# Optimization experiments

Hardware: AMD Instinct MI355X
Metric: run time of the kernel (lower is better)

## Reference

```python
import jax, jax.numpy as jnp
import numpy as np

EPS = 1e-08


def setup_inputs() -> dict:
    key = jax.random.key(0)
    k1, k2 = jax.random.split(key)
    z = jax.random.normal(k1, (32, 768, 32, 32), dtype=jnp.float32)
    memory = jax.random.normal(k2, (512, 768), dtype=jnp.float32)
    return {"z": z, "memory": memory}


def _l2_normalize(x, axis=-1, eps=1e-12):
    # Matches torch F.normalize(dim=-1): x / max(||x||, eps)
    n = jnp.sqrt(jnp.sum(x * x, axis=axis, keepdims=True))
    return x / jnp.maximum(n, eps)


def reference(z, memory):
    B, C, H, W = z.shape
    M = memory.shape[0]
    # (B, C, H, W) -> (B, H*W, C)
    z_flat = jnp.transpose(z, (0, 2, 3, 1)).reshape(B, H * W, C)
    z_norm = _l2_normalize(z_flat)
    mem_norm = _l2_normalize(memory)
    # cosine-similarity scores: (B, N, M)
    scores = jnp.einsum('bnc,mc->bnm', z_norm, mem_norm)
    w = jax.nn.softmax(scores, axis=-1)
    lam = 1.0 / M
    # hard-shrink sparsification: relu(w - lam) * w / (|w - lam| + eps)
    d = w - lam
    attn_w = jax.nn.relu(d) * w / (jnp.abs(d) + EPS)
    attn_w = attn_w / (jnp.sum(attn_w, axis=-1, keepdims=True) + EPS)
    # weighted readout against the RAW (un-normalized) memory
    z_hat_flat = jnp.einsum('bnm,mc->bnc', attn_w, memory)
    z_hat = jnp.transpose(z_hat_flat.reshape(B, H, W, C), (0, 3, 1, 2))
    return (z_hat, attn_w)
```

## Files before the change

### kernel.cpp

```cpp
#include <hip/hip_runtime.h>
#include <hip/hip_bf16.h>
#include <math.h>

typedef short short8 __attribute__((ext_vector_type(8)));
typedef float f32x4 __attribute__((ext_vector_type(4)));
typedef _Float16 f16x8 __attribute__((ext_vector_type(8)));

#define CC 768
#define NN 1024
#define RR 32768
#define MM 512
#define ZSTRIDE 786432
#define OUT_ATTN_OFF 25165824
#define SPLIT_SC 2048.0f
#define INV_SC   (1.0f / 2048.0f)

static __device__ __forceinline__ short f2bf(float f) {
    __hip_bfloat16 h = __float2bfloat16(f);
    return *reinterpret_cast<short*>(&h);
}

static __device__ __forceinline__ double fast_exp_neg(double x) {
    const double LOG2E = 1.4426950408889634074;
    const double LN2   = 0.6931471805599453094;
    const double MAGIC = 6755399441055744.0;
    double t = x * LOG2E;
    double c = t + MAGIC;
    double n = c - MAGIC;
    int ni = (int)__double2loint(c);
    double g = (t - n) * LN2;
    double r = 2.505210838544172e-08;
    r = fma(r, g, 2.755731922398589e-07);
    r = fma(r, g, 2.7557319223985893e-06);
    r = fma(r, g, 2.48015873015873e-05);
    r = fma(r, g, 1.984126984126984e-04);
    r = fma(r, g, 1.388888888888889e-03);
    r = fma(r, g, 8.333333333333333e-03);
    r = fma(r, g, 4.1666666666666664e-02);
    r = fma(r, g, 1.6666666666666666e-01);
    r = fma(r, g, 0.5);
    r = fma(r, g, 1.0);
    r = fma(r, g, 1.0);
    double sc = __hiloint2double((1023 + ni) << 20, 0);
    return r * sc;
}

static __device__ __forceinline__ double fast_rcp(double x) {
    double r = (double)(1.0f / (float)x);
    r = r * (2.0 - x * r);
    r = r * (2.0 - x * r);
    return r;
}

__global__ __launch_bounds__(256) void prep_mem_kernel(const float* __restrict__ memory,
                                                       _Float16* __restrict__ mem_h,
                                                       _Float16* __restrict__ mem_L,
                                                       short* __restrict__ memT_bf) {
    int m = blockIdx.x;
    int t = threadIdx.x;
    double ss = 0.0;
    for (int c = t; c < CC; c += 256) {
        float v = memory[m * CC + c];
        ss += (double)v * (double)v;
    }
    #pragma unroll
    for (int off = 32; off > 0; off >>= 1) ss += __shfl_xor(ss, off);
    __shared__ double red[4];
    __shared__ double invs;
    if ((t & 63) == 0) red[t >> 6] = ss;
    __syncthreads();
    if (t == 0) {
        double tot = red[0] + red[1] + red[2] + red[3];
        invs = 1.0 / fmax(sqrt(tot), 1e-12);
    }
    __syncthreads();
    float inv = (float)invs;
    for (int c = t; c < CC; c += 256) {
        float v  = memory[m * CC + c];
        float nv = v * inv;
        _Float16 h = (_Float16)nv;
        float r1 = nv - (float)h;
        mem_h[m * CC + c] = h;
        mem_L[m * CC + c] = (_Float16)(r1 * SPLIT_SC);
        memT_bf[c * MM + m] = f2bf(v);
    }
}

#define SWZ(row_, k_) ((((row_) << 5) + (k_)) ^ (((row_) & 7) << 3))
__global__ __launch_bounds__(512, 4) void scores_gemm_kernel(const float* __restrict__ z,
                                                             const _Float16* __restrict__ mem_h,
                                                             const _Float16* __restrict__ mem_L,
                                                             float* __restrict__ out_scores,
                                                             double* __restrict__ zinv_ws) {
    __shared__ _Float16 AT[2][2][4096];
    __shared__ _Float16 BT[2][2][4096];
    __shared__ double ssred[512];

    const int t    = threadIdx.x;
    const int lane = t & 63;
    const int wv   = t >> 6;
    const int lrow = lane & 15;
    const int gk   = lane >> 4;
    const int wr   = wv >> 1, wc = wv & 1;
    const int d = blockIdx.x;
    const int colblk = (d >> 3) & 3;
    const int rowblk = (d & 7) | ((d >> 5) << 3);
    const int row0 = rowblk * 128;
    const int b    = row0 >> 10;
    const int n0   = row0 & 1023;
    const int cB0  = colblk * 128;

    const int an  = t & 127;
    const int ak8 = (t >> 7) * 8;
    const float* zA = z + (size_t)b * ZSTRIDE + n0 + an;
    const int bc = t >> 2;
    const int kc = (t & 3) * 8;
    const _Float16* mhB = mem_h + (size_t)(cB0 + bc) * CC + kc;
    const _Float16* mLB = mem_L + (size_t)(cB0 + bc) * CC + kc;

    double ss = 0.0;
    f32x4 am[2][4], ax[2][4];
    #pragma unroll
    for (int fc = 0; fc < 2; ++fc)
        #pragma unroll
        for (int fn = 0; fn < 4; ++fn) {
            am[fc][fn] = (f32x4){0.f, 0.f, 0.f, 0.f};
            ax[fc][fn] = (f32x4){0.f, 0.f, 0.f, 0.f};
        }

    #define LOADS(kt_, av_, bh_, bl_)                                          \
        do {                                                                   \
            _Pragma("unroll")                                                  \
            for (int j = 0; j < 8; ++j)                                        \
                av_[j] = zA[(size_t)((kt_) * 32 + ak8 + j) * NN];              \
            bh_ = *reinterpret_cast<const f16x8*>(mhB + (kt_) * 32);           \
            bl_ = *reinterpret_cast<const f16x8*>(mLB + (kt_) * 32);           \
        } while (0)

    #define WRITES(bb_, av_, bh_, bl_)                                         \
        do {                                                                   \
            f16x8 h8, l8;                                                      \
            _Pragma("unroll")                                                  \
            for (int j = 0; j < 8; ++j) {                                      \
                float v = av_[j];                                              \
                ss = fma((double)v, (double)v, ss);                            \
                _Float16 h = (_Float16)v;                                      \
                h8[j] = h;                                                     \
                l8[j] = (_Float16)((v - (float)h) * SPLIT_SC);                 \
            }                                                                  \
            *reinterpret_cast<f16x8*>(&AT[bb_][0][SWZ(an, ak8)]) = h8;         \
            *reinterpret_cast<f16x8*>(&AT[bb_][1][SWZ(an, ak8)]) = l8;         \
            *reinterpret_cast<f16x8*>(&BT[bb_][0][SWZ(bc, kc)])  = bh_;        \
            *reinterpret_cast<f16x8*>(&BT[bb_][1][SWZ(bc, kc)])  = bl_;        \
        } while (0)

    {
        float av[8]; f16x8 bh8, bl8;
        LOADS(0, av, bh8, bl8);
        WRITES(0, av, bh8, bl8);
    }
    __syncthreads();

    #pragma unroll 1
    for (int kt = 0; kt < 24; ++kt) {
        const int cur = kt & 1;
        float av[8]; f16x8 bh8, bl8;
        if (kt < 23) LOADS(kt + 1, av, bh8, bl8);

        f16x8 ah[2], aL[2];
        #pragma unroll
        for (int fc = 0; fc < 2; ++fc) {
            ah[fc] = *reinterpret_cast<const f16x8*>(&AT[cur][0][SWZ(wr * 32 + fc * 16 + lrow, gk * 8)]);
            aL[fc] = *reinterpret_cast<const f16x8*>(&AT[cur][1][SWZ(wr * 32 + fc * 16 + lrow, gk * 8)]);
        }
        f16x8 bh[4], bL[4];
        #pragma unroll
        for (int fn = 0; fn < 4; ++fn) {
            bh[fn] = *reinterpret_cast<const f16x8*>(&BT[cur][0][SWZ(wc * 64 + fn * 16 + lrow, gk * 8)]);
            bL[fn] = *reinterpret_cast<const f16x8*>(&BT[cur][1][SWZ(wc * 64 + fn * 16 + lrow, gk * 8)]);
        }
        #pragma unroll
        for (int fn = 0; fn < 4; ++fn)
            #pragma unroll
            for (int fc = 0; fc < 2; ++fc) {
                am[fc][fn] = __builtin_amdgcn_mfma_f32_16x16x32_f16(ah[fc], bh[fn], am[fc][fn], 0, 0, 0);
                ax[fc][fn] = __builtin_amdgcn_mfma_f32_16x16x32_f16(aL[fc], bh[fn], ax[fc][fn], 0, 0, 0);
                ax[fc][fn] = __builtin_amdgcn_mfma_f32_16x16x32_f16(ah[fc], bL[fn], ax[fc][fn], 0, 0, 0);
            }

        if (kt < 23) WRITES(cur ^ 1, av, bh8, bl8);
        __syncthreads();
    }
    #undef LOADS
    #undef WRITES

    #pragma unroll
    for (int fc = 0; fc < 2; ++fc)
        #pragma unroll
        for (int fn = 0; fn < 4; ++fn)
            #pragma unroll
            for (int rg = 0; rg < 4; ++rg) {
                int row = row0 + wr * 32 + fc * 16 + gk * 4 + rg;
                int col = cB0 + wc * 64 + fn * 16 + lrow;
                out_scores[(size_t)row * MM + col] = am[fc][fn][rg] + ax[fc][fn][rg] * INV_SC;
            }

    ssred[t] = ss;
    __syncthreads();
    if (colblk == 0 && t < 128) {
        double tot = ssred[t] + ssred[t + 128] + ssred[t + 256] + ssred[t + 384];
        zinv_ws[row0 + t] = 1.0 / fmax(sqrt(tot), 1e-12);
    }
}
#undef SWZ

__global__ __launch_bounds__(256) void epilogue_kernel(float* __restrict__ attn,
                                                       const double* __restrict__ zinv_ws) {
    const int t    = threadIdx.x;
    const int lane = t & 63;
    const int wv   = t >> 6;
    const int row0 = blockIdx.x * 64;

    #pragma unroll 1
    for (int i = 0; i < 16; ++i) {
        int row = row0 + wv * 16 + i;
        double zi = zinv_ws[row];
        float* rp = attn + (size_t)row * MM;
        f32x4 x0 = *reinterpret_cast<const f32x4*>(&rp[lane * 4]);
        f32x4 x1 = *reinterpret_cast<const f32x4*>(&rp[256 + lane * 4]);
        double s0 = (double)x0[0] * zi, s1 = (double)x0[1] * zi;
        double s2 = (double)x0[2] * zi, s3 = (double)x0[3] * zi;
        double s4 = (double)x1[0] * zi, s5 = (double)x1[1] * zi;
        double s6 = (double)x1[2] * zi, s7 = (double)x1[3] * zi;
        double mx = fmax(fmax(fmax(s0, s1), fmax(s2, s3)),
                         fmax(fmax(s4, s5), fmax(s6, s7)));
        #pragma unroll
        for (int off = 32; off > 0; off >>= 1) mx = fmax(mx, __shfl_xor(mx, off));
        double p0 = fast_exp_neg(s0 - mx), p1 = fast_exp_neg(s1 - mx);
        double p2 = fast_exp_neg(s2 - mx), p3 = fast_exp_neg(s3 - mx);
        double p4 = fast_exp_neg(s4 - mx), p5 = fast_exp_neg(s5 - mx);
        double p6 = fast_exp_neg(s6 - mx), p7 = fast_exp_neg(s7 - mx);
        double Z = ((p0 + p1) + (p2 + p3)) + ((p4 + p5) + (p6 + p7));
        #pragma unroll
        for (int off = 32; off > 0; off >>= 1) Z += __shfl_xor(Z, off);
        double iZ = fast_rcp(Z);
        const double LAM = 1.0 / 512.0;
        double w0 = p0 * iZ, w1 = p1 * iZ, w2 = p2 * iZ, w3 = p3 * iZ;
        double w4 = p4 * iZ, w5 = p5 * iZ, w6 = p6 * iZ, w7 = p7 * iZ;
        double d0 = w0 - LAM, d1 = w1 - LAM, d2 = w2 - LAM, d3 = w3 - LAM;
        double d4 = w4 - LAM, d5 = w5 - LAM, d6 = w6 - LAM, d7 = w7 - LAM;
        double e0 = (d0 > 0.0 ? d0 : 0.0) * w0 * fast_rcp(fabs(d0) + 1e-8);
        double e1 = (d1 > 0.0 ? d1 : 0.0) * w1 * fast_rcp(fabs(d1) + 1e-8);
        double e2 = (d2 > 0.0 ? d2 : 0.0) * w2 * fast_rcp(fabs(d2) + 1e-8);
        double e3 = (d3 > 0.0 ? d3 : 0.0) * w3 * fast_rcp(fabs(d3) + 1e-8);
        double e4 = (d4 > 0.0 ? d4 : 0.0) * w4 * fast_rcp(fabs(d4) + 1e-8);
        double e5 = (d5 > 0.0 ? d5 : 0.0) * w5 * fast_rcp(fabs(d5) + 1e-8);
        double e6 = (d6 > 0.0 ? d6 : 0.0) * w6 * fast_rcp(fabs(d6) + 1e-8);
        double e7 = (d7 > 0.0 ? d7 : 0.0) * w7 * fast_rcp(fabs(d7) + 1e-8);
        double S = ((e0 + e1) + (e2 + e3)) + ((e4 + e5) + (e6 + e7));
        #pragma unroll
        for (int off = 32; off > 0; off >>= 1) S += __shfl_xor(S, off);
        double rinv = fast_rcp(S + 1e-8);
        f32x4 o0 = { (float)(e0 * rinv), (float)(e1 * rinv),
                     (float)(e2 * rinv), (float)(e3 * rinv) };
        f32x4 o1 = { (float)(e4 * rinv), (float)(e5 * rinv),
                     (float)(e6 * rinv), (float)(e7 * rinv) };
        *reinterpret_cast<f32x4*>(&rp[lane * 4])       = o0;
        *reinterpret_cast<f32x4*>(&rp[256 + lane * 4]) = o1;
    }
}

__global__ __launch_bounds__(256) void readout_kernel(const short* __restrict__ memT_bf,
                                                      const float* __restrict__ attn,
                                                      float* __restrict__ out) {
    __shared__ short At[64][40];
    __shared__ short Bt[128][40];
    int t = threadIdx.x;
    const int d  = blockIdx.x;
    const int xs = d & 7;
    const int hi = d >> 3;
    const int c0idx  = hi % 12;
    const int rowmid = hi / 12;
    const int rb128  = xs | (rowmid << 3);
    int c0     = c0idx * 64;
    int rowblk = rb128 * 128;
    int b  = rowblk >> 10;
    int nb = rowblk & 1023;
    int lane = t & 63, wv = t >> 6;

    f32x4 acc[4][2];
    #pragma unroll
    for (int fc = 0; fc < 4; ++fc)
        #pragma unroll
        for (int fn = 0; fn < 2; ++fn) acc[fc][fn] = (f32x4){0.f, 0.f, 0.f, 0.f};

    for (int m0 = 0; m0 < MM; m0 += 32) {
        __syncthreads();
        {
            int r = t >> 2, ko = (t & 3) * 8;
            short8 v = *reinterpret_cast<const short8*>(&memT_bf[(c0 + r) * MM + m0 + ko]);
            *reinterpret_cast<short8*>(&At[r][ko]) = v;
        }
        {
            int r = t >> 1, ko = (t & 1) * 16;
            const f32x4* src = reinterpret_cast<const f32x4*>(
                &attn[(size_t)(rowblk + r) * MM + m0 + ko]);
            f32x4 v0 = src[0], v1 = src[1], v2 = src[2], v3 = src[3];
            short8 s0 = { f2bf(v0[0]), f2bf(v0[1]), f2bf(v0[2]), f2bf(v0[3]),
                          f2bf(v1[0]), f2bf(v1[1]), f2bf(v1[2]), f2bf(v1[3]) };
            short8 s1 = { f2bf(v2[0]), f2bf(v2[1]), f2bf(v2[2]), f2bf(v2[3]),
                          f2bf(v3[0]), f2bf(v3[1]), f2bf(v3[2]), f2bf(v3[3]) };
            *reinterpret_cast<short8*>(&Bt[r][ko])     = s0;
            *reinterpret_cast<short8*>(&Bt[r][ko + 8]) = s1;
        }
        __syncthreads();
        short8 af[4], bfr[2];
        #pragma unroll
        for (int fc = 0; fc < 4; ++fc)
            af[fc] = *reinterpret_cast<const short8*>(&At[fc * 16 + (lane & 15)][(lane >> 4) * 8]);
        #pragma unroll
        for (int fn = 0; fn < 2; ++fn)
            bfr[fn] = *reinterpret_cast<const short8*>(&Bt[wv * 32 + fn * 16 + (lane & 15)][(lane >> 4) * 8]);
        #pragma unroll
        for (int fc = 0; fc < 4; ++fc)
            #pragma unroll
            for (int fn = 0; fn < 2; ++fn)
                acc[fc][fn] = __builtin_amdgcn_mfma_f32_16x16x32_bf16(af[fc], bfr[fn], acc[fc][fn], 0, 0, 0);
    }

    int cg = lane >> 4, cl = lane & 15;
    #pragma unroll
    for (int fc = 0; fc < 4; ++fc)
        #pragma unroll
        for (int fn = 0; fn < 2; ++fn)
            #pragma unroll
            for (int reg = 0; reg < 4; ++reg) {
                int c = c0 + fc * 16 + cg * 4 + reg;
                int n = nb + wv * 32 + fn * 16 + cl;
                out[(size_t)b * ZSTRIDE + (size_t)c * NN + n] = acc[fc][fn][reg];
            }
}

extern "C" void kernel_launch(void* const* d_in, const int* in_sizes, int n_in,
                              void* d_out, int out_size, void* d_ws, size_t ws_size,
                              hipStream_t stream) {
    const float* z      = (const float*)d_in[0];
    const float* memory = (const float*)d_in[1];
    float* out      = (float*)d_out;
    float* out_attn = out + OUT_ATTN_OFF;

    char* wsb = (char*)d_ws;
    _Float16* mem_h   = (_Float16*)wsb;
    _Float16* mem_L   = (_Float16*)(wsb + 786432);
    short*    memT_bf = (short*)(wsb + 1572864);
    double*   zinv_ws = (double*)(wsb + 2359296);

    prep_mem_kernel<<<512, 256, 0, stream>>>(memory, mem_h, mem_L, memT_bf);
    scores_gemm_kernel<<<1024, 512, 0, stream>>>(z, mem_h, mem_L, out_attn, zinv_ws);
    epilogue_kernel<<<RR / 64, 256, 0, stream>>>(out_attn, zinv_ws);
    readout_kernel<<<3072, 256, 0, stream>>>(memT_bf, out_attn, out);
}
```

Baseline: 207.7 us.

## Enlarge per-wave register tiles in scores and readout GEMMs with fewer threads

The scores GEMM drops from 512 to 256 threads per block, so each wave computes a 64x64 tile instead of 32x64, and each thread loads twice as many z and memory elements per stage. The readout kernel doubles its channel tile to 128 and uses a 2x2 wave layout with 4x4 MFMA fragments, which halves the grid and lets each fragment loaded from LDS feed more MFMAs. The aim is less LDS traffic per MFMA and less block overhead. The cost is more accumulator registers per thread, which may lower occupancy or cause spills, especially in the split-precision scores kernel that keeps two accumulator sets.

After: 197.3 us. 5.0% less time.

```diff
diff --git a/kernel.cpp b/kernel.cpp
--- a/kernel.cpp
+++ b/kernel.cpp
@@ -87,14 +87,14 @@
 }
 
 #define SWZ(row_, k_) ((((row_) << 5) + (k_)) ^ (((row_) & 7) << 3))
-__global__ __launch_bounds__(512, 4) void scores_gemm_kernel(const float* __restrict__ z,
+__global__ __launch_bounds__(256, 2) void scores_gemm_kernel(const float* __restrict__ z,
                                                              const _Float16* __restrict__ mem_h,
                                                              const _Float16* __restrict__ mem_L,
                                                              float* __restrict__ out_scores,
                                                              double* __restrict__ zinv_ws) {
     __shared__ _Float16 AT[2][2][4096];
     __shared__ _Float16 BT[2][2][4096];
-    __shared__ double ssred[512];
+    __shared__ double ssred[256];
 
     const int t    = threadIdx.x;
     const int lane = t & 63;
@@ -110,18 +110,18 @@
     const int n0   = row0 & 1023;
     const int cB0  = colblk * 128;
 
-    const int an  = t & 127;
-    const int ak8 = (t >> 7) * 8;
+    const int an   = t & 127;
+    const int ak16 = (t >> 7) * 16;
     const float* zA = z + (size_t)b * ZSTRIDE + n0 + an;
-    const int bc = t >> 2;
-    const int kc = (t & 3) * 8;
+    const int bc = t >> 1;
+    const int kc = (t & 1) * 16;
     const _Float16* mhB = mem_h + (size_t)(cB0 + bc) * CC + kc;
     const _Float16* mLB = mem_L + (size_t)(cB0 + bc) * CC + kc;
 
     double ss = 0.0;
-    f32x4 am[2][4], ax[2][4];
-    #pragma unroll
-    for (int fc = 0; fc < 2; ++fc)
+    f32x4 am[4][4], ax[4][4];
+    #pragma unroll
+    for (int fc = 0; fc < 4; ++fc)
         #pragma unroll
         for (int fn = 0; fn < 4; ++fn) {
             am[fc][fn] = (f32x4){0.f, 0.f, 0.f, 0.f};
@@ -131,31 +131,45 @@
     #define LOADS(kt_, av_, bh_, bl_)                                          \
         do {                                                                   \
             _Pragma("unroll")                                                  \
-            for (int j = 0; j < 8; ++j)                                        \
-                av_[j] = zA[(size_t)((kt_) * 32 + ak8 + j) * NN];              \
-            bh_ = *reinterpret_cast<const f16x8*>(mhB + (kt_) * 32);           \
-            bl_ = *reinterpret_cast<const f16x8*>(mLB + (kt_) * 32);           \
+            for (int j = 0; j < 16; ++j)                                       \
+                av_[j] = zA[(size_t)((kt_) * 32 + ak16 + j) * NN];             \
+            bh_[0] = *reinterpret_cast<const f16x8*>(mhB + (kt_) * 32);        \
+            bh_[1] = *reinterpret_cast<const f16x8*>(mhB + (kt_) * 32 + 8);    \
+            bl_[0] = *reinterpret_cast<const f16x8*>(mLB + (kt_) * 32);        \
+            bl_[1] = *reinterpret_cast<const f16x8*>(mLB + (kt_) * 32 + 8);    \
         } while (0)
 
     #define WRITES(bb_, av_, bh_, bl_)                                         \
         do {                                                                   \
-            f16x8 h8, l8;                                                      \
+            f16x8 h8a, l8a, h8b, l8b;                                          \
             _Pragma("unroll")                                                  \
             for (int j = 0; j < 8; ++j) {                                      \
                 float v = av_[j];                                              \
                 ss = fma((double)v, (double)v, ss);                            \
                 _Float16 h = (_Float16)v;                                      \
-                h8[j] = h;                                                     \
-                l8[j] = (_Float16)((v - (float)h) * SPLIT_SC);                 \
+                h8a[j] = h;                                                    \
+                l8a[j] = (_Float16)((v - (float)h) * SPLIT_SC);                \
             }                                                                  \
-            *reinterpret_cast<f16x8*>(&AT[bb_][0][SWZ(an, ak8)]) = h8;         \
-            *reinterpret_cast<f16x8*>(&AT[bb_][1][SWZ(an, ak8)]) = l8;         \
-            *reinterpret_cast<f16x8*>(&BT[bb_][0][SWZ(bc, kc)])  = bh_;        \
-            *reinterpret_cast<f16x8*>(&BT[bb_][1][SWZ(bc, kc)])  = bl_;        \
+            _Pragma("unroll")                                                  \
+            for (int j = 0; j < 8; ++j) {                                      \
+                float v = av_[8 + j];                                          \
+                ss = fma((double)v, (double)v, ss);                            \
+                _Float16 h = (_Float16)v;                                      \
+                h8b[j] = h;                                                    \
+                l8b[j] = (_Float16)((v - (float)h) * SPLIT_SC);                \
+            }                                                                  \
+            *reinterpret_cast<f16x8*>(&AT[bb_][0][SWZ(an, ak16)])     = h8a;   \
+            *reinterpret_cast<f16x8*>(&AT[bb_][0][SWZ(an, ak16 + 8)]) = h8b;   \
+            *reinterpret_cast<f16x8*>(&AT[bb_][1][SWZ(an, ak16)])     = l8a;   \
+            *reinterpret_cast<f16x8*>(&AT[bb_][1][SWZ(an, ak16 + 8)]) = l8b;   \
+            *reinterpret_cast<f16x8*>(&BT[bb_][0][SWZ(bc, kc)])       = bh_[0];\
+            *reinterpret_cast<f16x8*>(&BT[bb_][0][SWZ(bc, kc + 8)])   = bh_[1];\
+            *reinterpret_cast<f16x8*>(&BT[bb_][1][SWZ(bc, kc)])       = bl_[0];\
+            *reinterpret_cast<f16x8*>(&BT[bb_][1][SWZ(bc, kc + 8)])   = bl_[1];\
         } while (0)
 
     {
-        float av[8]; f16x8 bh8, bl8;
+        float av[16]; f16x8 bh8[2], bl8[2];
         LOADS(0, av, bh8, bl8);
         WRITES(0, av, bh8, bl8);
     }
@@ -164,14 +178,14 @@
     #pragma unroll 1
     for (int kt = 0; kt < 24; ++kt) {
         const int cur = kt & 1;
-        float av[8]; f16x8 bh8, bl8;
+        float av[16]; f16x8 bh8[2], bl8[2];
         if (kt < 23) LOADS(kt + 1, av, bh8, bl8);
 
-        f16x8 ah[2], aL[2];
-        #pragma unroll
-        for (int fc = 0; fc < 2; ++fc) {
-            ah[fc] = *reinterpret_cast<const f16x8*>(&AT[cur][0][SWZ(wr * 32 + fc * 16 + lrow, gk * 8)]);
-            aL[fc] = *reinterpret_cast<const f16x8*>(&AT[cur][1][SWZ(wr * 32 + fc * 16 + lrow, gk * 8)]);
+        f16x8 ah[4], aL[4];
+        #pragma unroll
+        for (int fc = 0; fc < 4; ++fc) {
+            ah[fc] = *reinterpret_cast<const f16x8*>(&AT[cur][0][SWZ(wr * 64 + fc * 16 + lrow, gk * 8)]);
+            aL[fc] = *reinterpret_cast<const f16x8*>(&AT[cur][1][SWZ(wr * 64 + fc * 16 + lrow, gk * 8)]);
         }
         f16x8 bh[4], bL[4];
         #pragma unroll
@@ -182,7 +196,7 @@
         #pragma unroll
         for (int fn = 0; fn < 4; ++fn)
             #pragma unroll
-            for (int fc = 0; fc < 2; ++fc) {
+            for (int fc = 0; fc < 4; ++fc) {
                 am[fc][fn] = __builtin_amdgcn_mfma_f32_16x16x32_f16(ah[fc], bh[fn], am[fc][fn], 0, 0, 0);
                 ax[fc][fn] = __builtin_amdgcn_mfma_f32_16x16x32_f16(aL[fc], bh[fn], ax[fc][fn], 0, 0, 0);
                 ax[fc][fn] = __builtin_amdgcn_mfma_f32_16x16x32_f16(ah[fc], bL[fn], ax[fc][fn], 0, 0, 0);
@@ -195,12 +209,12 @@
     #undef WRITES
 
     #pragma unroll
-    for (int fc = 0; fc < 2; ++fc)
+    for (int fc = 0; fc < 4; ++fc)
         #pragma unroll
         for (int fn = 0; fn < 4; ++fn)
             #pragma unroll
             for (int rg = 0; rg < 4; ++rg) {
-                int row = row0 + wr * 32 + fc * 16 + gk * 4 + rg;
+                int row = row0 + wr * 64 + fc * 16 + gk * 4 + rg;
                 int col = cB0 + wc * 64 + fn * 16 + lrow;
                 out_scores[(size_t)row * MM + col] = am[fc][fn][rg] + ax[fc][fn][rg] * INV_SC;
             }
@@ -208,7 +222,7 @@
     ssred[t] = ss;
     __syncthreads();
     if (colblk == 0 && t < 128) {
-        double tot = ssred[t] + ssred[t + 128] + ssred[t + 256] + ssred[t + 384];
+        double tot = ssred[t] + ssred[t + 128];
         zinv_ws[row0 + t] = 1.0 / fmax(sqrt(tot), 1e-12);
     }
 }
@@ -270,73 +284,77 @@
     }
 }
 
-__global__ __launch_bounds__(256) void readout_kernel(const short* __restrict__ memT_bf,
-                                                      const float* __restrict__ attn,
-                                                      float* __restrict__ out) {
-    __shared__ short At[64][40];
+__global__ __launch_bounds__(256, 3) void readout_kernel(const short* __restrict__ memT_bf,
+                                                         const float* __restrict__ attn,
+                                                         float* __restrict__ out) {
+    __shared__ short At[128][40];
     __shared__ short Bt[128][40];
-    int t = threadIdx.x;
+    const int t = threadIdx.x;
     const int d  = blockIdx.x;
     const int xs = d & 7;
     const int hi = d >> 3;
-    const int c0idx  = hi % 12;
-    const int rowmid = hi / 12;
-    const int rb128  = xs | (rowmid << 3);
-    int c0     = c0idx * 64;
-    int rowblk = rb128 * 128;
-    int b  = rowblk >> 10;
-    int nb = rowblk & 1023;
-    int lane = t & 63, wv = t >> 6;
-
-    f32x4 acc[4][2];
+    const int c0idx  = hi % 6;
+    const int rowmid = hi / 6;
+    const int rb     = xs | (rowmid << 3);
+    const int c0     = c0idx * 128;
+    const int rowblk = rb * 128;
+    const int b  = rowblk >> 10;
+    const int nb = rowblk & 1023;
+    const int lane = t & 63, wv = t >> 6;
+    const int wcr = wv >> 1, wcc = wv & 1;
+    const int lrow = lane & 15, gk = lane >> 4;
+
+    f32x4 acc[4][4];
     #pragma unroll
     for (int fc = 0; fc < 4; ++fc)
         #pragma unroll
-        for (int fn = 0; fn < 2; ++fn) acc[fc][fn] = (f32x4){0.f, 0.f, 0.f, 0.f};
+        for (int fn = 0; fn < 4; ++fn) acc[fc][fn] = (f32x4){0.f, 0.f, 0.f, 0.f};
+
+    const int sr = t >> 1;
+    const int ko = (t & 1) * 16;
 
     for (int m0 = 0; m0 < MM; m0 += 32) {
         __syncthreads();
         {
-            int r = t >> 2, ko = (t & 3) * 8;
-            short8 v = *reinterpret_cast<const short8*>(&memT_bf[(c0 + r) * MM + m0 + ko]);
-            *reinterpret_cast<short8*>(&At[r][ko]) = v;
+            const short8* src = reinterpret_cast<const short8*>(
+                &memT_bf[(c0 + sr) * MM + m0 + ko]);
+            *reinterpret_cast<short8*>(&At[sr][ko])     = src[0];
+            *reinterpret_cast<short8*>(&At[sr][ko + 8]) = src[1];
         }
         {
-            int r = t >> 1, ko = (t & 1) * 16;
             const f32x4* src = reinterpret_cast<const f32x4*>(
-                &attn[(size_t)(rowblk + r) * MM + m0 + ko]);
+                &attn[(size_t)(rowblk + sr) * MM + m0 + ko]);
             f32x4 v0 = src[0], v1 = src[1], v2 = src[2], v3 = src[3];
             short8 s0 = { f2bf(v0[0]), f2bf(v0[1]), f2bf(v0[2]), f2bf(v0[3]),
                           f2bf(v1[0]), f2bf(v1[1]), f2bf(v1[2]), f2bf(v1[3]) };
             short8 s1 = { f2bf(v2[0]), f2bf(v2[1]), f2bf(v2[2]), f2bf(v2[3]),
                           f2bf(v3[0]), f2bf(v3[1]), f2bf(v3[2]), f2bf(v3[3]) };
-            *reinterpret_cast<short8*>(&Bt[r][ko])     = s0;
-            *reinterpret_cast<short8*>(&Bt[r][ko + 8]) = s1;
+            *reinterpret_cast<short8*>(&Bt[sr][ko])     = s0;
+            *reinterpret_cast<short8*>(&Bt[sr][ko + 8]) = s1;
         }
         __syncthreads();
-        short8 af[4], bfr[2];
+        short8 af[4], bf[4];
         #pragma unroll
         for (int fc = 0; fc < 4; ++fc)
-            af[fc] = *reinterpret_cast<const short8*>(&At[fc * 16 + (lane & 15)][(lane >> 4) * 8]);
-        #pragma unroll
-        for (int fn = 0; fn < 2; ++fn)
-            bfr[fn] = *reinterpret_cast<const short8*>(&Bt[wv * 32 + fn * 16 + (lane & 15)][(lane >> 4) * 8]);
+            af[fc] = *reinterpret_cast<const short8*>(&At[wcr * 64 + fc * 16 + lrow][gk * 8]);
+        #pragma unroll
+        for (int fn = 0; fn < 4; ++fn)
+            bf[fn] = *reinterpret_cast<const short8*>(&Bt[wcc * 64 + fn * 16 + lrow][gk * 8]);
         #pragma unroll
         for (int fc = 0; fc < 4; ++fc)
             #pragma unroll
-            for (int fn = 0; fn < 2; ++fn)
-                acc[fc][fn] = __builtin_amdgcn_mfma_f32_16x16x32_bf16(af[fc], bfr[fn], acc[fc][fn], 0, 0, 0);
-    }
-
-    int cg = lane >> 4, cl = lane & 15;
+            for (int fn = 0; fn < 4; ++fn)
+                acc[fc][fn] = __builtin_amdgcn_mfma_f32_16x16x32_bf16(af[fc], bf[fn], acc[fc][fn], 0, 0, 0);
+    }
+
     #pragma unroll
     for (int fc = 0; fc < 4; ++fc)
         #pragma unroll
-        for (int fn = 0; fn < 2; ++fn)
+        for (int fn = 0; fn < 4; ++fn)
             #pragma unroll
             for (int reg = 0; reg < 4; ++reg) {
-                int c = c0 + fc * 16 + cg * 4 + reg;
-                int n = nb + wv * 32 + fn * 16 + cl;
+                int c = c0 + wcr * 64 + fc * 16 + gk * 4 + reg;
+                int n = nb + wcc * 64 + fn * 16 + lrow;
                 out[(size_t)b * ZSTRIDE + (size_t)c * NN + n] = acc[fc][fn][reg];
             }
 }
@@ -356,7 +374,7 @@
     double*   zinv_ws = (double*)(wsb + 2359296);
 
     prep_mem_kernel<<<512, 256, 0, stream>>>(memory, mem_h, mem_L, memT_bf);
-    scores_gemm_kernel<<<1024, 512, 0, stream>>>(z, mem_h, mem_L, out_attn, zinv_ws);
+    scores_gemm_kernel<<<1024, 256, 0, stream>>>(z, mem_h, mem_L, out_attn, zinv_ws);
     epilogue_kernel<<<RR / 64, 256, 0, stream>>>(out_attn, zinv_ws);
-    readout_kernel<<<3072, 256, 0, stream>>>(memT_bf, out_attn, out);
-}
+    readout_kernel<<<1536, 256, 0, stream>>>(memT_bf, out_attn, out);
+}
```
